# Optimization experiments

Measured on AMD Instinct MI355X. Metric: run time of the kernel, lower is better.

## Reference

```python
import jax, jax.numpy as jnp
import numpy as np

B, T, I, H, L = 32, 1024, 1024, 1024, 3


def setup_inputs() -> dict:
    key = jax.random.key(0)
    ks = jax.random.split(key, 8)
    sc_in = 1.0 / np.sqrt(I)
    sc_h = 1.0 / np.sqrt(H)
    return {
        "x": jax.random.normal(ks[0], (B, T, I), dtype=jnp.float32),
        "s0": jnp.zeros((B, H), dtype=jnp.float32),
        "w_h": jax.random.normal(ks[1], (I, H), dtype=jnp.float32) * sc_in,
        "w_t": jax.random.normal(ks[2], (I, H), dtype=jnp.float32) * sc_in,
        "w_c": jax.random.normal(ks[3], (I, H), dtype=jnp.float32) * sc_in,
        "Rh": jax.random.normal(ks[4], (L, H, H), dtype=jnp.float32) * sc_h,
        "Rt": jax.random.normal(ks[5], (L, H, H), dtype=jnp.float32) * sc_h,
        "Rc": jax.random.normal(ks[6], (L, H, H), dtype=jnp.float32) * sc_h,
        "bh": jnp.zeros((L, H), dtype=jnp.float32),
        "bt": jnp.zeros((L, H), dtype=jnp.float32),
        "bc": jnp.zeros((L, H), dtype=jnp.float32),
    }


def reference(x, s0, w_h, w_t, w_c, Rh, Rt, Rc, bh, bt, bc):
    # x: [B, T, I]; s0: [B, H]. Dropout prob = 0 -> identity.
    num_layers = Rh.shape[0]

    def step(s, x_t):
        # Input projections only feed layer 0 (as in the torch code).
        whx = x_t @ w_h  # [B, H]
        wtx = x_t @ w_t
        wcx = x_t @ w_c
        for l in range(num_layers):
            h_in = (whx if l == 0 else 0.0) + s @ Rh[l].T + bh[l]
            t_in = (wtx if l == 0 else 0.0) + s @ Rt[l].T + bt[l]
            c_in = (wcx if l == 0 else 0.0) + s @ Rc[l].T + bc[l]
            h = jnp.tanh(h_in)
            t = jax.nn.sigmoid(t_in)
            c = jax.nn.sigmoid(c_in)
            s = h * t + s * c
        return s, s

    x_tbi = jnp.swapaxes(x, 0, 1)  # [T, B, I] for scan over time
    s_T, outs = jax.lax.scan(step, s0, x_tbi)
    return jnp.swapaxes(outs, 0, 1), s_T  # ([B, T, H], [B, H])
```

## Files before the change

kernel.cpp:

```cpp
#include <hip/hip_runtime.h>
#include <hip/hip_bf16.h>

static constexpr int Bb = 32;
static constexpr int Tt = 1024;
static constexpr int Ii = 1024;
static constexpr int Hh = 1024;
static constexpr int NWG = 256;

typedef float f4 __attribute__((ext_vector_type(4)));

static constexpr int LDS_WORDS = 36 * 1024 + 4 * 12 * 32;
static constexpr int LDS_BYTES = LDS_WORDS * 4;

template <typename PT> __device__ __forceinline__ float pt_to_f(PT v);
template <> __device__ __forceinline__ float pt_to_f<float>(float v) { return v; }
template <> __device__ __forceinline__ float pt_to_f<__hip_bfloat16>(__hip_bfloat16 v) { return __bfloat162float(v); }

template <typename PT> __device__ __forceinline__ PT f_to_pt(float v);
template <> __device__ __forceinline__ float f_to_pt<float>(float v) { return v; }
template <> __device__ __forceinline__ __hip_bfloat16 f_to_pt<__hip_bfloat16>(float v) { return __float2bfloat16(v); }

#define SGLD(dst, p, lit) \
    asm volatile("global_load_dwordx4 %0, %1, off offset:" lit " sc0 sc1" : "=v"(dst) : "v"(p))
#define GB(sv, p, a,b,c,d2,e,f,g2,h) \
    SGLD(sv[0],p,a); SGLD(sv[1],p,b); SGLD(sv[2],p,c); SGLD(sv[3],p,d2); \
    SGLD(sv[4],p,e); SGLD(sv[5],p,f); SGLD(sv[6],p,g2); SGLD(sv[7],p,h)
#define VWAIT(n) do { asm volatile("s_waitcnt vmcnt(" #n ")" ::: "memory"); \
                      __builtin_amdgcn_sched_barrier(0); } while (0)

template <typename PT>
__global__ __launch_bounds__(256, 2) void proj_gemm(
    const float* __restrict__ X, const float* __restrict__ Wh,
    const float* __restrict__ Wt, const float* __restrict__ Wc,
    PT* __restrict__ P2)
{
    __shared__ float smem[4160];
    float* As = smem;
    float* Bs = smem + 1088;

    const int tid = threadIdx.x;
    const int tx = tid & 15, ty = tid >> 4;
    const int col0 = blockIdx.x * 64;
    const int t0 = blockIdx.y * 2;

    float acc[3][4][4];
#pragma unroll
    for (int g = 0; g < 3; ++g)
#pragma unroll
        for (int mm = 0; mm < 4; ++mm)
#pragma unroll
            for (int nn = 0; nn < 4; ++nn) acc[g][mm][nn] = 0.f;

    const int lm = tid >> 2, lk4 = (tid & 3) * 4;
    const float* aptr = X + ((size_t)(lm & 31) * Tt + (t0 + (lm >> 5))) * Ii + lk4;
    const int bk = tid >> 4, bn4 = (tid & 15) * 4;

    for (int k0 = 0; k0 < Ii; k0 += 16) {
        float4 av = *(const float4*)(aptr + k0);
        As[(lk4 + 0) * 68 + lm] = av.x;
        As[(lk4 + 1) * 68 + lm] = av.y;
        As[(lk4 + 2) * 68 + lm] = av.z;
        As[(lk4 + 3) * 68 + lm] = av.w;
        *(float4*)&Bs[0 * 1024 + bk * 64 + bn4] = *(const float4*)(Wh + (size_t)(k0 + bk) * Hh + col0 + bn4);
        *(float4*)&Bs[1 * 1024 + bk * 64 + bn4] = *(const float4*)(Wt + (size_t)(k0 + bk) * Hh + col0 + bn4);
        *(float4*)&Bs[2 * 1024 + bk * 64 + bn4] = *(const float4*)(Wc + (size_t)(k0 + bk) * Hh + col0 + bn4);
        __syncthreads();
#pragma unroll
        for (int k = 0; k < 16; ++k) {
            float4 a = *(const float4*)&As[k * 68 + ty * 4];
            float a_[4] = {a.x, a.y, a.z, a.w};
#pragma unroll
            for (int g = 0; g < 3; ++g) {
                float4 b = *(const float4*)&Bs[g * 1024 + k * 64 + tx * 4];
                float b_[4] = {b.x, b.y, b.z, b.w};
#pragma unroll
                for (int mm = 0; mm < 4; ++mm)
#pragma unroll
                    for (int nn = 0; nn < 4; ++nn)
                        acc[g][mm][nn] += a_[mm] * b_[nn];
            }
        }
        __syncthreads();
    }

    float* E = smem;
    const int b4 = (tid & 7) * 4;
#pragma unroll 1
    for (int g = 0; g < 3; ++g) {
        __syncthreads();
#pragma unroll
        for (int mm = 0; mm < 4; ++mm)
#pragma unroll
            for (int nn = 0; nn < 4; ++nn)
                E[(ty * 4 + mm) * 65 + tx * 4 + nn] = acc[g][mm][nn];
        __syncthreads();
        PT* dst = P2 + (size_t)g * Tt * Hh * Bb;
#pragma unroll
        for (int it = 0; it < 4; ++it) {
            const int line = (tid >> 3) + it * 32;
            const int tt = line >> 6, hh = line & 63;
            const float o0 = E[(tt * 32 + b4 + 0) * 65 + hh];
            const float o1 = E[(tt * 32 + b4 + 1) * 65 + hh];
            const float o2 = E[(tt * 32 + b4 + 2) * 65 + hh];
            const float o3 = E[(tt * 32 + b4 + 3) * 65 + hh];
            PT* d = dst + ((size_t)(t0 + tt) * Hh + col0 + hh) * Bb + b4;
            d[0] = f_to_pt<PT>(o0); d[1] = f_to_pt<PT>(o1);
            d[2] = f_to_pt<PT>(o2); d[3] = f_to_pt<PT>(o3);
        }
    }
}

__global__ void init_k(const float* __restrict__ s0, float* __restrict__ sbuf,
                       unsigned* __restrict__ flags)
{
    const int i = blockIdx.x * 256 + threadIdx.x;
    if (i < Bb * Hh) { const int b = i >> 10, h = i & 1023; sbuf[h * 32 + b] = s0[i]; }
    if (i < 256) flags[i] = 0;
}

template <typename ST>
__global__ __launch_bounds__(256) void out_transpose(
    const ST* __restrict__ shist, float* __restrict__ out, float* __restrict__ sT)
{
    __shared__ float tile[128 * 33];
    const int tid = threadIdx.x;
    const int h0 = blockIdx.x * 128;
    const int t = blockIdx.y;
    const ST* src = shist + ((size_t)t * Hh + h0) * Bb;
#pragma unroll
    for (int e = 0; e < 16; ++e) {
        const int idx = e * 256 + tid;
        tile[(idx >> 5) * 33 + (idx & 31)] = pt_to_f<ST>(src[idx]);
    }
    __syncthreads();
    const int hi = tid & 31, bq = tid >> 5;
#pragma unroll
    for (int e = 0; e < 4; ++e) {
        const int b = bq + e * 8;
        float4 v;
        v.x = tile[(hi * 4 + 0) * 33 + b];
        v.y = tile[(hi * 4 + 1) * 33 + b];
        v.z = tile[(hi * 4 + 2) * 33 + b];
        v.w = tile[(hi * 4 + 3) * 33 + b];
        *(float4*)(out + ((size_t)b * Tt + t) * Hh + h0 + hi * 4) = v;
        if (t == Tt - 1) *(float4*)(sT + (size_t)b * Hh + h0 + hi * 4) = v;
    }
}

template <typename PT, typename ST, bool DIRECT>
__global__ __launch_bounds__(256, 1) void rhn_recur(
    const float* __restrict__ Rh, const float* __restrict__ Rt,
    const float* __restrict__ Rc, const float* __restrict__ bh,
    const float* __restrict__ bt, const float* __restrict__ bc,
    const PT* __restrict__ P2, float* __restrict__ sbuf,
    unsigned* __restrict__ flags, ST* __restrict__ shist,
    float* __restrict__ out, float* __restrict__ sT)
{
    extern __shared__ float lds[];
    float* part = lds + 36 * 1024;

    const int g = blockIdx.x;
    const int tid = threadIdx.x;

    {
        const int k4 = tid * 4;
        const int sk = k4 ^ (((k4 >> 5) & 7) << 2);
#pragma unroll 1
        for (int j = 0; j < 36; ++j) {
            const int l = j / 12;
            const int rem = j - l * 12;
            const int gt = rem >> 2;
            const int q = rem & 3;
            const int h = (q << 8) | g;
            const float* src = (gt == 0 ? Rh : (gt == 1 ? Rt : Rc)) + ((size_t)l * Hh + h) * Hh;
            *(float4*)&lds[(j << 10) | sk] = *(const float4*)(src + k4);
        }
    }
    __syncthreads();

    const int ks = tid >> 3;
    const int b0 = (tid & 7) << 2;
    const int q8 = ks & 7;
    const int wv = tid >> 6;
    const int ub = tid & 31;
    const int uqc = (tid >> 5) & 3;
    const int uhc = (uqc << 8) | g;

    int o2[8];
#pragma unroll
    for (int c = 0; c < 8; ++c) o2[c] = ((c ^ q8) << 2);

    float brh[3], brt[3], brc[3];
#pragma unroll
    for (int l = 0; l < 3; ++l) {
        brh[l] = bh[l * Hh + uhc];
        brt[l] = bt[l * Hh + uhc];
        brc[l] = bc[l * Hh + uhc];
    }

    float so_reg = sbuf[uhc * 32 + ub];

    const float* sr = sbuf;
    float* sw = sbuf + Hh * Bb;

#pragma unroll 1
    for (int t = 0; t < Tt; ++t) {
#pragma unroll 1
        for (int l = 0; l < 3; ++l) {
            float pv0 = 0.f, pv1 = 0.f, pv2 = 0.f;
            if (l == 0 && tid < 128) {
                const size_t pb = ((size_t)t * Hh + uhc) * Bb + ub;
                pv0 = pt_to_f<PT>(P2[pb]);
                pv1 = pt_to_f<PT>(P2[(size_t)Tt * Hh * Bb + pb]);
                pv2 = pt_to_f<PT>(P2[2 * (size_t)Tt * Hh * Bb + pb]);
            }

            const float* sA = sr + (ks << 5) * 32 + b0;
            const float* rp = lds + l * 12288 + (ks << 5);

            f4 accv[12];
#pragma unroll
            for (int jj = 0; jj < 12; ++jj) accv[jj] = (f4){0.f, 0.f, 0.f, 0.f};

            f4 sv0[8], sv1[8];
            GB(sv0, sA, "0","128","256","384","512","640","768","896");
            GB(sv1, sA, "1024","1152","1280","1408","1536","1664","1792","1920");
            VWAIT(8);
#pragma unroll
            for (int jj = 0; jj < 12; ++jj) {
                const f4 r0 = *(const f4*)(rp + jj * 1024 + o2[0]);
                const f4 r1 = *(const f4*)(rp + jj * 1024 + o2[1]);
                f4 a = accv[jj];
                a += sv0[0] * r0[0]; a += sv0[1] * r0[1]; a += sv0[2] * r0[2]; a += sv0[3] * r0[3];
                a += sv0[4] * r1[0]; a += sv0[5] * r1[1]; a += sv0[6] * r1[2]; a += sv0[7] * r1[3];
                accv[jj] = a;
            }
            GB(sv0, sA, "2048","2176","2304","2432","2560","2688","2816","2944");
            VWAIT(8);
#pragma unroll
            for (int jj = 0; jj < 12; ++jj) {
                const f4 r0 = *(const f4*)(rp + jj * 1024 + o2[2]);
                const f4 r1 = *(const f4*)(rp + jj * 1024 + o2[3]);
                f4 a = accv[jj];
                a += sv1[0] * r0[0]; a += sv1[1] * r0[1]; a += sv1[2] * r0[2]; a += sv1[3] * r0[3];
                a += sv1[4] * r1[0]; a += sv1[5] * r1[1]; a += sv1[6] * r1[2]; a += sv1[7] * r1[3];
                accv[jj] = a;
            }
            GB(sv1, sA, "3072","3200","3328","3456","3584","3712","3840","3968");
            VWAIT(8);
#pragma unroll
            for (int jj = 0; jj < 12; ++jj) {
                const f4 r0 = *(const f4*)(rp + jj * 1024 + o2[4]);
                const f4 r1 = *(const f4*)(rp + jj * 1024 + o2[5]);
                f4 a = accv[jj];
                a += sv0[0] * r0[0]; a += sv0[1] * r0[1]; a += sv0[2] * r0[2]; a += sv0[3] * r0[3];
                a += sv0[4] * r1[0]; a += sv0[5] * r1[1]; a += sv0[6] * r1[2]; a += sv0[7] * r1[3];
                accv[jj] = a;
            }
            VWAIT(0);
#pragma unroll
            for (int jj = 0; jj < 12; ++jj) {
                const f4 r0 = *(const f4*)(rp + jj * 1024 + o2[6]);
                const f4 r1 = *(const f4*)(rp + jj * 1024 + o2[7]);
                f4 a = accv[jj];
                a += sv1[0] * r0[0]; a += sv1[1] * r0[1]; a += sv1[2] * r0[2]; a += sv1[3] * r0[3];
                a += sv1[4] * r1[0]; a += sv1[5] * r1[1]; a += sv1[6] * r1[2]; a += sv1[7] * r1[3];
                accv[jj] = a;
            }

#pragma unroll
            for (int jj = 0; jj < 12; ++jj) {
#pragma unroll
                for (int st = 8; st <= 32; st <<= 1) {
                    accv[jj][0] += __shfl_xor(accv[jj][0], st);
                    accv[jj][1] += __shfl_xor(accv[jj][1], st);
                    accv[jj][2] += __shfl_xor(accv[jj][2], st);
                    accv[jj][3] += __shfl_xor(accv[jj][3], st);
                }
            }
            f4 s1 = accv[0];
#pragma unroll
            for (int j2 = 1; j2 < 8; ++j2) if (q8 == j2) s1 = accv[j2];
            f4 s2 = accv[8];
#pragma unroll
            for (int j2 = 1; j2 < 4; ++j2) if (q8 == j2) s2 = accv[8 + j2];
            *(f4*)&part[(wv * 12 + q8) * 32 + b0] = s1;
            if (q8 < 4) *(f4*)&part[(wv * 12 + 8 + q8) * 32 + b0] = s2;
            __syncthreads();

            if (tid < 128) {
                float vals[3];
#pragma unroll
                for (int gt = 0; gt < 3; ++gt) {
                    const int jl = (gt << 2) + uqc;
                    vals[gt] = part[jl * 32 + ub] + part[(12 + jl) * 32 + ub]
                             + part[(24 + jl) * 32 + ub] + part[(36 + jl) * 32 + ub];
                }
                float bb0, bb1, bb2;
                if (l == 0)      { bb0 = brh[0]; bb1 = brt[0]; bb2 = brc[0]; }
                else if (l == 1) { bb0 = brh[1]; bb1 = brt[1]; bb2 = brc[1]; }
                else             { bb0 = brh[2]; bb1 = brt[2]; bb2 = brc[2]; }
                vals[0] += bb0; vals[1] += bb1; vals[2] += bb2;
                if (l == 0) { vals[0] += pv0; vals[1] += pv1; vals[2] += pv2; }
                const float hv = 1.f - 2.f / (1.f + __expf(2.f * vals[0]));
                const float tv = 1.f / (1.f + __expf(-vals[1]));
                const float cv = 1.f / (1.f + __expf(-vals[2]));
                const float sn = hv * tv + so_reg * cv;
                so_reg = sn;
                __hip_atomic_store(&sw[uhc * 32 + ub], sn, __ATOMIC_RELAXED, __HIP_MEMORY_SCOPE_AGENT);
                if (!DIRECT) {
                    if (l == 2) shist[((size_t)t * Hh + uhc) * Bb + ub] = f_to_pt<ST>(sn);
                } else {
                    if (l == 2) {
                        out[((size_t)ub * Tt + t) * Hh + uhc] = sn;
                        if (t == Tt - 1) sT[(size_t)ub * Hh + uhc] = sn;
                    }
                }
            }

            const unsigned ph = (unsigned)(t * 3 + l + 1);
            __syncthreads();
            if (tid == 0)
                __hip_atomic_store(&flags[g], ph, __ATOMIC_RELAXED, __HIP_MEMORY_SCOPE_AGENT);
            if (tid < 64) {
                for (;;) {
                    const unsigned v0 = __hip_atomic_load(&flags[tid],       __ATOMIC_RELAXED, __HIP_MEMORY_SCOPE_AGENT);
                    const unsigned v1 = __hip_atomic_load(&flags[tid + 64],  __ATOMIC_RELAXED, __HIP_MEMORY_SCOPE_AGENT);
                    const unsigned v2 = __hip_atomic_load(&flags[tid + 128], __ATOMIC_RELAXED, __HIP_MEMORY_SCOPE_AGENT);
                    const unsigned v3 = __hip_atomic_load(&flags[tid + 192], __ATOMIC_RELAXED, __HIP_MEMORY_SCOPE_AGENT);
                    if (__all((int)((v0 >= ph) & (v1 >= ph) & (v2 >= ph) & (v3 >= ph)))) break;
                    __builtin_amdgcn_s_sleep(2);
                }
            }
            __syncthreads();

            float* tmp = const_cast<float*>(sr);
            sr = sw;
            sw = tmp;
        }
    }
}

extern "C" void kernel_launch(void* const* d_in, const int* in_sizes, int n_in,
                              void* d_out, int out_size, void* d_ws, size_t ws_size,
                              hipStream_t stream)
{
    (void)in_sizes; (void)n_in; (void)out_size;
    const float* x  = (const float*)d_in[0];
    const float* s0 = (const float*)d_in[1];
    const float* wh = (const float*)d_in[2];
    const float* wt = (const float*)d_in[3];
    const float* wc = (const float*)d_in[4];
    const float* Rh = (const float*)d_in[5];
    const float* Rt = (const float*)d_in[6];
    const float* Rc = (const float*)d_in[7];
    const float* bh = (const float*)d_in[8];
    const float* bt = (const float*)d_in[9];
    const float* bc = (const float*)d_in[10];

    float* out = (float*)d_out;
    float* sT  = out + (size_t)Bb * Tt * Hh;

    const size_t THB  = (size_t)Tt * Hh * Bb;
    const size_t p2f  = 3 * THB * 4, p2h = 3 * THB * 2;
    const size_t shf  = THB * 4,     shh = THB * 2;
    const size_t tail = 2 * (size_t)Hh * Bb * 4 + 4096;

    char* w = (char*)d_ws;
    float* sbuf;
    unsigned* flags;

    auto finish = [&](float* sbufp, unsigned* flagsp) {
        init_k<<<128, 256, 0, stream>>>(s0, sbufp, flagsp);
    };

    if (ws_size >= p2f + shf + tail) {
        float* P2 = (float*)w;
        float* shist = (float*)(w + p2f);
        sbuf = (float*)(w + p2f + shf);
        flags = (unsigned*)((char*)sbuf + 2 * (size_t)Hh * Bb * 4);
        proj_gemm<float><<<dim3(16, 512), 256, 0, stream>>>(x, wh, wt, wc, P2);
        finish(sbuf, flags);
        hipFuncSetAttribute(reinterpret_cast<const void*>(rhn_recur<float, float, false>),
                            hipFuncAttributeMaxDynamicSharedMemorySize, LDS_BYTES);
        void* args[] = {(void*)&Rh, (void*)&Rt, (void*)&Rc, (void*)&bh, (void*)&bt, (void*)&bc,
                        (void*)&P2, (void*)&sbuf, (void*)&flags, (void*)&shist, (void*)&out, (void*)&sT};
        hipLaunchCooperativeKernel(reinterpret_cast<void*>(rhn_recur<float, float, false>),
                                   dim3(NWG), dim3(256), args, LDS_BYTES, stream);
        out_transpose<float><<<dim3(8, 1024), 256, 0, stream>>>(shist, out, sT);
    } else if (ws_size >= p2h + shf + tail) {
        __hip_bfloat16* P2 = (__hip_bfloat16*)w;
        float* shist = (float*)(w + p2h);
        sbuf = (float*)(w + p2h + shf);
        flags = (unsigned*)((char*)sbuf + 2 * (size_t)Hh * Bb * 4);
        proj_gemm<__hip_bfloat16><<<dim3(16, 512), 256, 0, stream>>>(x, wh, wt, wc, P2);
        finish(sbuf, flags);
        hipFuncSetAttribute(reinterpret_cast<const void*>(rhn_recur<__hip_bfloat16, float, false>),
                            hipFuncAttributeMaxDynamicSharedMemorySize, LDS_BYTES);
        void* args[] = {(void*)&Rh, (void*)&Rt, (void*)&Rc, (void*)&bh, (void*)&bt, (void*)&bc,
                        (void*)&P2, (void*)&sbuf, (void*)&flags, (void*)&shist, (void*)&out, (void*)&sT};
        hipLaunchCooperativeKernel(reinterpret_cast<void*>(rhn_recur<__hip_bfloat16, float, false>),
                                   dim3(NWG), dim3(256), args, LDS_BYTES, stream);
        out_transpose<float><<<dim3(8, 1024), 256, 0, stream>>>(shist, out, sT);
    } else if (ws_size >= p2h + shh + tail) {
        __hip_bfloat16* P2 = (__hip_bfloat16*)w;
        __hip_bfloat16* shist = (__hip_bfloat16*)(w + p2h);
        sbuf = (float*)(w + p2h + shh);
        flags = (unsigned*)((char*)sbuf + 2 * (size_t)Hh * Bb * 4);
        proj_gemm<__hip_bfloat16><<<dim3(16, 512), 256, 0, stream>>>(x, wh, wt, wc, P2);
        finish(sbuf, flags);
        hipFuncSetAttribute(reinterpret_cast<const void*>(rhn_recur<__hip_bfloat16, __hip_bfloat16, false>),
                            hipFuncAttributeMaxDynamicSharedMemorySize, LDS_BYTES);
        void* args[] = {(void*)&Rh, (void*)&Rt, (void*)&Rc, (void*)&bh, (void*)&bt, (void*)&bc,
                        (void*)&P2, (void*)&sbuf, (void*)&flags, (void*)&shist, (void*)&out, (void*)&sT};
        hipLaunchCooperativeKernel(reinterpret_cast<void*>(rhn_recur<__hip_bfloat16, __hip_bfloat16, false>),
                                   dim3(NWG), dim3(256), args, LDS_BYTES, stream);
        out_transpose<__hip_bfloat16><<<dim3(8, 1024), 256, 0, stream>>>(shist, out, sT);
    } else {
        __hip_bfloat16* P2 = (__hip_bfloat16*)w;
        sbuf = (float*)(w + p2h);
        flags = (unsigned*)((char*)sbuf + 2 * (size_t)Hh * Bb * 4);
        float* shist = sbuf;
        proj_gemm<__hip_bfloat16><<<dim3(16, 512), 256, 0, stream>>>(x, wh, wt, wc, P2);
        finish(sbuf, flags);
        hipFuncSetAttribute(reinterpret_cast<const void*>(rhn_recur<__hip_bfloat16, float, true>),
                            hipFuncAttributeMaxDynamicSharedMemorySize, LDS_BYTES);
        void* args[] = {(void*)&Rh, (void*)&Rt, (void*)&Rc, (void*)&bh, (void*)&bt, (void*)&bc,
                        (void*)&P2, (void*)&sbuf, (void*)&flags, (void*)&shist, (void*)&out, (void*)&sT};
        hipLaunchCooperativeKernel(reinterpret_cast<void*>(rhn_recur<__hip_bfloat16, float, true>),
                                   dim3(NWG), dim3(256), args, LDS_BYTES, stream);
    }
}
```

Baseline: 34.86 ms.

## Replace ping-pong state buffer with write-once ring so reads can use cached loads

The two-slot swapped state buffer becomes a ring holding one slot per layer-step, so each slot is written once and never overwritten. That lets the recurrent state loads drop the sc0 sc1 cache-bypass bits and use normal cached loads. The ring also serves as the output history, removing the separate shist buffer and the per-step history store. It costs a much larger workspace and depends on cached reads of freshly written slots staying coherent across workgroups.

```diff
diff --git a/kernel.cpp b/kernel.cpp
--- a/kernel.cpp
+++ b/kernel.cpp
@@ -7,6 +7,9 @@
 static constexpr int Hh = 1024;
 static constexpr int NWG = 256;
 
+static constexpr int SLOT_E = Hh * Bb;
+static constexpr int NSLOT  = 3 * Tt + 1;
+
 typedef float f4 __attribute__((ext_vector_type(4)));
 
 static constexpr int LDS_WORDS = 36 * 1024 + 4 * 12 * 32;
@@ -20,11 +23,11 @@
 template <> __device__ __forceinline__ float f_to_pt<float>(float v) { return v; }
 template <> __device__ __forceinline__ __hip_bfloat16 f_to_pt<__hip_bfloat16>(float v) { return __float2bfloat16(v); }
 
-#define SGLD(dst, p, lit) \
-    asm volatile("global_load_dwordx4 %0, %1, off offset:" lit " sc0 sc1" : "=v"(dst) : "v"(p))
+#define CGLD(dst, p, lit) \
+    asm volatile("global_load_dwordx4 %0, %1, off offset:" lit : "=v"(dst) : "v"(p))
 #define GB(sv, p, a,b,c,d2,e,f,g2,h) \
-    SGLD(sv[0],p,a); SGLD(sv[1],p,b); SGLD(sv[2],p,c); SGLD(sv[3],p,d2); \
-    SGLD(sv[4],p,e); SGLD(sv[5],p,f); SGLD(sv[6],p,g2); SGLD(sv[7],p,h)
+    CGLD(sv[0],p,a); CGLD(sv[1],p,b); CGLD(sv[2],p,c); CGLD(sv[3],p,d2); \
+    CGLD(sv[4],p,e); CGLD(sv[5],p,f); CGLD(sv[6],p,g2); CGLD(sv[7],p,h)
 #define VWAIT(n) do { asm volatile("s_waitcnt vmcnt(" #n ")" ::: "memory"); \
                       __builtin_amdgcn_sched_barrier(0); } while (0)
 
@@ -101,36 +104,37 @@
             const int tt = line >> 6, hh = line & 63;
             const float o0 = E[(tt * 32 + b4 + 0) * 65 + hh];
             const float o1 = E[(tt * 32 + b4 + 1) * 65 + hh];
-            const float o2 = E[(tt * 32 + b4 + 2) * 65 + hh];
+            const float o2v = E[(tt * 32 + b4 + 2) * 65 + hh];
             const float o3 = E[(tt * 32 + b4 + 3) * 65 + hh];
             PT* d = dst + ((size_t)(t0 + tt) * Hh + col0 + hh) * Bb + b4;
             d[0] = f_to_pt<PT>(o0); d[1] = f_to_pt<PT>(o1);
-            d[2] = f_to_pt<PT>(o2); d[3] = f_to_pt<PT>(o3);
+            d[2] = f_to_pt<PT>(o2v); d[3] = f_to_pt<PT>(o3);
         }
     }
 }
 
-__global__ void init_k(const float* __restrict__ s0, float* __restrict__ sbuf,
+template <typename RT>
+__global__ void init_k(const float* __restrict__ s0, RT* __restrict__ ring0,
                        unsigned* __restrict__ flags)
 {
     const int i = blockIdx.x * 256 + threadIdx.x;
-    if (i < Bb * Hh) { const int b = i >> 10, h = i & 1023; sbuf[h * 32 + b] = s0[i]; }
+    if (i < Bb * Hh) { const int b = i >> 10, h = i & 1023; ring0[h * 32 + b] = f_to_pt<RT>(s0[i]); }
     if (i < 256) flags[i] = 0;
 }
 
-template <typename ST>
+template <typename RT>
 __global__ __launch_bounds__(256) void out_transpose(
-    const ST* __restrict__ shist, float* __restrict__ out, float* __restrict__ sT)
+    const RT* __restrict__ ring, float* __restrict__ out, float* __restrict__ sT)
 {
     __shared__ float tile[128 * 33];
     const int tid = threadIdx.x;
     const int h0 = blockIdx.x * 128;
     const int t = blockIdx.y;
-    const ST* src = shist + ((size_t)t * Hh + h0) * Bb;
+    const RT* src = ring + (size_t)(3 * t + 3) * SLOT_E + h0 * 32;
 #pragma unroll
     for (int e = 0; e < 16; ++e) {
         const int idx = e * 256 + tid;
-        tile[(idx >> 5) * 33 + (idx & 31)] = pt_to_f<ST>(src[idx]);
+        tile[(idx >> 5) * 33 + (idx & 31)] = pt_to_f<RT>(src[idx]);
     }
     __syncthreads();
     const int hi = tid & 31, bq = tid >> 5;
@@ -147,14 +151,13 @@
     }
 }
 
-template <typename PT, typename ST, bool DIRECT>
+template <typename PT, typename RT>
 __global__ __launch_bounds__(256, 1) void rhn_recur(
     const float* __restrict__ Rh, const float* __restrict__ Rt,
     const float* __restrict__ Rc, const float* __restrict__ bh,
     const float* __restrict__ bt, const float* __restrict__ bc,
-    const PT* __restrict__ P2, float* __restrict__ sbuf,
-    unsigned* __restrict__ flags, ST* __restrict__ shist,
-    float* __restrict__ out, float* __restrict__ sT)
+    const PT* __restrict__ P2, RT* __restrict__ ring,
+    unsigned* __restrict__ flags)
 {
     extern __shared__ float lds[];
     float* part = lds + 36 * 1024;
@@ -198,15 +201,14 @@
         brc[l] = bc[l * Hh + uhc];
     }
 
-    float so_reg = sbuf[uhc * 32 + ub];
-
-    const float* sr = sbuf;
-    float* sw = sbuf + Hh * Bb;
+    float so_reg = pt_to_f<RT>(ring[uhc * 32 + ub]);
 
 #pragma unroll 1
     for (int t = 0; t < Tt; ++t) {
 #pragma unroll 1
         for (int l = 0; l < 3; ++l) {
+            const int p = t * 3 + l;
+
             float pv0 = 0.f, pv1 = 0.f, pv2 = 0.f;
             if (l == 0 && tid < 128) {
                 const size_t pb = ((size_t)t * Hh + uhc) * Bb + ub;
@@ -215,57 +217,82 @@
                 pv2 = pt_to_f<PT>(P2[2 * (size_t)Tt * Hh * Bb + pb]);
             }
 
-            const float* sA = sr + (ks << 5) * 32 + b0;
             const float* rp = lds + l * 12288 + (ks << 5);
 
             f4 accv[12];
 #pragma unroll
             for (int jj = 0; jj < 12; ++jj) accv[jj] = (f4){0.f, 0.f, 0.f, 0.f};
 
-            f4 sv0[8], sv1[8];
-            GB(sv0, sA, "0","128","256","384","512","640","768","896");
-            GB(sv1, sA, "1024","1152","1280","1408","1536","1664","1792","1920");
-            VWAIT(8);
-#pragma unroll
-            for (int jj = 0; jj < 12; ++jj) {
-                const f4 r0 = *(const f4*)(rp + jj * 1024 + o2[0]);
-                const f4 r1 = *(const f4*)(rp + jj * 1024 + o2[1]);
-                f4 a = accv[jj];
-                a += sv0[0] * r0[0]; a += sv0[1] * r0[1]; a += sv0[2] * r0[2]; a += sv0[3] * r0[3];
-                a += sv0[4] * r1[0]; a += sv0[5] * r1[1]; a += sv0[6] * r1[2]; a += sv0[7] * r1[3];
-                accv[jj] = a;
-            }
-            GB(sv0, sA, "2048","2176","2304","2432","2560","2688","2816","2944");
-            VWAIT(8);
-#pragma unroll
-            for (int jj = 0; jj < 12; ++jj) {
-                const f4 r0 = *(const f4*)(rp + jj * 1024 + o2[2]);
-                const f4 r1 = *(const f4*)(rp + jj * 1024 + o2[3]);
-                f4 a = accv[jj];
-                a += sv1[0] * r0[0]; a += sv1[1] * r0[1]; a += sv1[2] * r0[2]; a += sv1[3] * r0[3];
-                a += sv1[4] * r1[0]; a += sv1[5] * r1[1]; a += sv1[6] * r1[2]; a += sv1[7] * r1[3];
-                accv[jj] = a;
-            }
-            GB(sv1, sA, "3072","3200","3328","3456","3584","3712","3840","3968");
-            VWAIT(8);
-#pragma unroll
-            for (int jj = 0; jj < 12; ++jj) {
-                const f4 r0 = *(const f4*)(rp + jj * 1024 + o2[4]);
-                const f4 r1 = *(const f4*)(rp + jj * 1024 + o2[5]);
-                f4 a = accv[jj];
-                a += sv0[0] * r0[0]; a += sv0[1] * r0[1]; a += sv0[2] * r0[2]; a += sv0[3] * r0[3];
-                a += sv0[4] * r1[0]; a += sv0[5] * r1[1]; a += sv0[6] * r1[2]; a += sv0[7] * r1[3];
-                accv[jj] = a;
-            }
-            VWAIT(0);
-#pragma unroll
-            for (int jj = 0; jj < 12; ++jj) {
-                const f4 r0 = *(const f4*)(rp + jj * 1024 + o2[6]);
-                const f4 r1 = *(const f4*)(rp + jj * 1024 + o2[7]);
-                f4 a = accv[jj];
-                a += sv1[0] * r0[0]; a += sv1[1] * r0[1]; a += sv1[2] * r0[2]; a += sv1[3] * r0[3];
-                a += sv1[4] * r1[0]; a += sv1[5] * r1[1]; a += sv1[6] * r1[2]; a += sv1[7] * r1[3];
-                accv[jj] = a;
+            if constexpr (sizeof(RT) == 4) {
+                const float* sA = (const float*)ring + (size_t)p * SLOT_E + (ks << 5) * 32 + b0;
+                f4 sv0[8], sv1[8];
+                GB(sv0, sA, "0","128","256","384","512","640","768","896");
+                GB(sv1, sA, "1024","1152","1280","1408","1536","1664","1792","1920");
+                VWAIT(8);
+#pragma unroll
+                for (int jj = 0; jj < 12; ++jj) {
+                    const f4 r0 = *(const f4*)(rp + jj * 1024 + o2[0]);
+                    const f4 r1 = *(const f4*)(rp + jj * 1024 + o2[1]);
+                    f4 a = accv[jj];
+                    a += sv0[0] * r0[0]; a += sv0[1] * r0[1]; a += sv0[2] * r0[2]; a += sv0[3] * r0[3];
+                    a += sv0[4] * r1[0]; a += sv0[5] * r1[1]; a += sv0[6] * r1[2]; a += sv0[7] * r1[3];
+                    accv[jj] = a;
+                }
+                GB(sv0, sA, "2048","2176","2304","2432","2560","2688","2816","2944");
+                VWAIT(8);
+#pragma unroll
+                for (int jj = 0; jj < 12; ++jj) {
+                    const f4 r0 = *(const f4*)(rp + jj * 1024 + o2[2]);
+                    const f4 r1 = *(const f4*)(rp + jj * 1024 + o2[3]);
+                    f4 a = accv[jj];
+                    a += sv1[0] * r0[0]; a += sv1[1] * r0[1]; a += sv1[2] * r0[2]; a += sv1[3] * r0[3];
+                    a += sv1[4] * r1[0]; a += sv1[5] * r1[1]; a += sv1[6] * r1[2]; a += sv1[7] * r1[3];
+                    accv[jj] = a;
+                }
+                GB(sv1, sA, "3072","3200","3328","3456","3584","3712","3840","3968");
+                VWAIT(8);
+#pragma unroll
+                for (int jj = 0; jj < 12; ++jj) {
+                    const f4 r0 = *(const f4*)(rp + jj * 1024 + o2[4]);
+                    const f4 r1 = *(const f4*)(rp + jj * 1024 + o2[5]);
+                    f4 a = accv[jj];
+                    a += sv0[0] * r0[0]; a += sv0[1] * r0[1]; a += sv0[2] * r0[2]; a += sv0[3] * r0[3];
+                    a += sv0[4] * r1[0]; a += sv0[5] * r1[1]; a += sv0[6] * r1[2]; a += sv0[7] * r1[3];
+                    accv[jj] = a;
+                }
+                VWAIT(0);
+#pragma unroll
+                for (int jj = 0; jj < 12; ++jj) {
+                    const f4 r0 = *(const f4*)(rp + jj * 1024 + o2[6]);
+                    const f4 r1 = *(const f4*)(rp + jj * 1024 + o2[7]);
+                    f4 a = accv[jj];
+                    a += sv1[0] * r0[0]; a += sv1[1] * r0[1]; a += sv1[2] * r0[2]; a += sv1[3] * r0[3];
+                    a += sv1[4] * r1[0]; a += sv1[5] * r1[1]; a += sv1[6] * r1[2]; a += sv1[7] * r1[3];
+                    accv[jj] = a;
+                }
+            } else {
+                const __hip_bfloat16* sIn = (const __hip_bfloat16*)ring + (size_t)p * SLOT_E + (ks << 5) * 32 + b0;
+#pragma unroll
+                for (int blk = 0; blk < 4; ++blk) {
+                    f4 sv[8];
+#pragma unroll
+                    for (int i = 0; i < 8; ++i) {
+                        const ushort4 u = *(const ushort4*)(sIn + (blk * 8 + i) * 32);
+                        sv[i][0] = __uint_as_float((unsigned)u.x << 16);
+                        sv[i][1] = __uint_as_float((unsigned)u.y << 16);
+                        sv[i][2] = __uint_as_float((unsigned)u.z << 16);
+                        sv[i][3] = __uint_as_float((unsigned)u.w << 16);
+                    }
+#pragma unroll
+                    for (int jj = 0; jj < 12; ++jj) {
+                        const f4 r0 = *(const f4*)(rp + jj * 1024 + o2[blk * 2]);
+                        const f4 r1 = *(const f4*)(rp + jj * 1024 + o2[blk * 2 + 1]);
+                        f4 a = accv[jj];
+                        a += sv[0] * r0[0]; a += sv[1] * r0[1]; a += sv[2] * r0[2]; a += sv[3] * r0[3];
+                        a += sv[4] * r1[0]; a += sv[5] * r1[1]; a += sv[6] * r1[2]; a += sv[7] * r1[3];
+                        accv[jj] = a;
+                    }
+                }
             }
 
 #pragma unroll
@@ -307,18 +334,17 @@
                 const float cv = 1.f / (1.f + __expf(-vals[2]));
                 const float sn = hv * tv + so_reg * cv;
                 so_reg = sn;
-                __hip_atomic_store(&sw[uhc * 32 + ub], sn, __ATOMIC_RELAXED, __HIP_MEMORY_SCOPE_AGENT);
-                if (!DIRECT) {
-                    if (l == 2) shist[((size_t)t * Hh + uhc) * Bb + ub] = f_to_pt<ST>(sn);
+                RT* wp = ring + (size_t)(p + 1) * SLOT_E + uhc * 32 + ub;
+                if constexpr (sizeof(RT) == 4) {
+                    __hip_atomic_store((float*)wp, sn, __ATOMIC_RELAXED, __HIP_MEMORY_SCOPE_AGENT);
                 } else {
-                    if (l == 2) {
-                        out[((size_t)ub * Tt + t) * Hh + uhc] = sn;
-                        if (t == Tt - 1) sT[(size_t)ub * Hh + uhc] = sn;
-                    }
-                }
-            }
-
-            const unsigned ph = (unsigned)(t * 3 + l + 1);
+                    __hip_bfloat16 b16 = __float2bfloat16(sn);
+                    __hip_atomic_store((unsigned short*)wp, *(unsigned short*)&b16,
+                                       __ATOMIC_RELAXED, __HIP_MEMORY_SCOPE_AGENT);
+                }
+            }
+
+            const unsigned ph = (unsigned)(p + 1);
             __syncthreads();
             if (tid == 0)
                 __hip_atomic_store(&flags[g], ph, __ATOMIC_RELAXED, __HIP_MEMORY_SCOPE_AGENT);
@@ -333,10 +359,6 @@
                 }
             }
             __syncthreads();
-
-            float* tmp = const_cast<float*>(sr);
-            sr = sw;
-            sw = tmp;
         }
     }
 }
@@ -363,71 +385,50 @@
 
     const size_t THB  = (size_t)Tt * Hh * Bb;
     const size_t p2f  = 3 * THB * 4, p2h = 3 * THB * 2;
-    const size_t shf  = THB * 4,     shh = THB * 2;
-    const size_t tail = 2 * (size_t)Hh * Bb * 4 + 4096;
+    const size_t ringF = (size_t)NSLOT * SLOT_E * 4;
+    const size_t ringH = (size_t)NSLOT * SLOT_E * 2;
+    const size_t tail = 4096;
 
     char* w = (char*)d_ws;
-    float* sbuf;
-    unsigned* flags;
-
-    auto finish = [&](float* sbufp, unsigned* flagsp) {
-        init_k<<<128, 256, 0, stream>>>(s0, sbufp, flagsp);
-    };
-
-    if (ws_size >= p2f + shf + tail) {
+
+    if (ws_size >= p2f + ringF + tail) {
         float* P2 = (float*)w;
-        float* shist = (float*)(w + p2f);
-        sbuf = (float*)(w + p2f + shf);
-        flags = (unsigned*)((char*)sbuf + 2 * (size_t)Hh * Bb * 4);
+        float* ring = (float*)(w + p2f);
+        unsigned* flags = (unsigned*)(w + p2f + ringF);
         proj_gemm<float><<<dim3(16, 512), 256, 0, stream>>>(x, wh, wt, wc, P2);
-        finish(sbuf, flags);
-        hipFuncSetAttribute(reinterpret_cast<const void*>(rhn_recur<float, float, false>),
+        init_k<float><<<128, 256, 0, stream>>>(s0, ring, flags);
+        hipFuncSetAttribute(reinterpret_cast<const void*>(rhn_recur<float, float>),
                             hipFuncAttributeMaxDynamicSharedMemorySize, LDS_BYTES);
         void* args[] = {(void*)&Rh, (void*)&Rt, (void*)&Rc, (void*)&bh, (void*)&bt, (void*)&bc,
-                        (void*)&P2, (void*)&sbuf, (void*)&flags, (void*)&shist, (void*)&out, (void*)&sT};
-        hipLaunchCooperativeKernel(reinterpret_cast<void*>(rhn_recur<float, float, false>),
+                        (void*)&P2, (void*)&ring, (void*)&flags};
+        hipLaunchCooperativeKernel(reinterpret_cast<void*>(rhn_recur<float, float>),
                                    dim3(NWG), dim3(256), args, LDS_BYTES, stream);
-        out_transpose<float><<<dim3(8, 1024), 256, 0, stream>>>(shist, out, sT);
-    } else if (ws_size >= p2h + shf + tail) {
+        out_transpose<float><<<dim3(8, 1024), 256, 0, stream>>>(ring, out, sT);
+    } else if (ws_size >= p2h + ringF + tail) {
         __hip_bfloat16* P2 = (__hip_bfloat16*)w;
-        float* shist = (float*)(w + p2h);
-        sbuf = (float*)(w + p2h + shf);
-        flags = (unsigned*)((char*)sbuf + 2 * (size_t)Hh * Bb * 4);
+        float* ring = (float*)(w + p2h);
+        unsigned* flags = (unsigned*)(w + p2h + ringF);
         proj_gemm<__hip_bfloat16><<<dim3(16, 512), 256, 0, stream>>>(x, wh, wt, wc, P2);
-        finish(sbuf, flags);
-        hipFuncSetAttribute(reinterpret_cast<const void*>(rhn_recur<__hip_bfloat16, float, false>),
+        init_k<float><<<128, 256, 0, stream>>>(s0, ring, flags);
+        hipFuncSetAttribute(reinterpret_cast<const void*>(rhn_recur<__hip_bfloat16, float>),
                             hipFuncAttributeMaxDynamicSharedMemorySize, LDS_BYTES);
         void* args[] = {(void*)&Rh, (void*)&Rt, (void*)&Rc, (void*)&bh, (void*)&bt, (void*)&bc,
-                        (void*)&P2, (void*)&sbuf, (void*)&flags, (void*)&shist, (void*)&out, (void*)&sT};
-        hipLaunchCooperativeKernel(reinterpret_cast<void*>(rhn_recur<__hip_bfloat16, float, false>),
+                        (void*)&P2, (void*)&ring, (void*)&flags};
+        hipLaunchCooperativeKernel(reinterpret_cast<void*>(rhn_recur<__hip_bfloat16, float>),
                                    dim3(NWG), dim3(256), args, LDS_BYTES, stream);
-        out_transpose<float><<<dim3(8, 1024), 256, 0, stream>>>(shist, out, sT);
-    } else if (ws_size >= p2h + shh + tail) {
+        out_transpose<float><<<dim3(8, 1024), 256, 0, stream>>>(ring, out, sT);
+    } else {
         __hip_bfloat16* P2 = (__hip_bfloat16*)w;
-        __hip_bfloat16* shist = (__hip_bfloat16*)(w + p2h);
-        sbuf = (float*)(w + p2h + shh);
-        flags = (unsigned*)((char*)sbuf + 2 * (size_t)Hh * Bb * 4);
+        __hip_bfloat16* ring = (__hip_bfloat16*)(w + p2h);
+        unsigned* flags = (unsigned*)(w + p2h + ringH);
         proj_gemm<__hip_bfloat16><<<dim3(16, 512), 256, 0, stream>>>(x, wh, wt, wc, P2);
-        finish(sbuf, flags);
-        hipFuncSetAttribute(reinterpret_cast<const void*>(rhn_recur<__hip_bfloat16, __hip_bfloat16, false>),
+        init_k<__hip_bfloat16><<<128, 256, 0, stream>>>(s0, ring, flags);
+        hipFuncSetAttribute(reinterpret_cast<const void*>(rhn_recur<__hip_bfloat16, __hip_bfloat16>),
                             hipFuncAttributeMaxDynamicSharedMemorySize, LDS_BYTES);
         void* args[] = {(void*)&Rh, (void*)&Rt, (void*)&Rc, (void*)&bh, (void*)&bt, (void*)&bc,
-                        (void*)&P2, (void*)&sbuf, (void*)&flags, (void*)&shist, (void*)&out, (void*)&sT};
-        hipLaunchCooperativeKernel(reinterpret_cast<void*>(rhn_recur<__hip_bfloat16, __hip_bfloat16, false>),
+                        (void*)&P2, (void*)&ring, (void*)&flags};
+        hipLaunchCooperativeKernel(reinterpret_cast<void*>(rhn_recur<__hip_bfloat16, __hip_bfloat16>),
                                    dim3(NWG), dim3(256), args, LDS_BYTES, stream);
-        out_transpose<__hip_bfloat16><<<dim3(8, 1024), 256, 0, stream>>>(shist, out, sT);
-    } else {
-        __hip_bfloat16* P2 = (__hip_bfloat16*)w;
-        sbuf = (float*)(w + p2h);
-        flags = (unsigned*)((char*)sbuf + 2 * (size_t)Hh * Bb * 4);
-        float* shist = sbuf;
-        proj_gemm<__hip_bfloat16><<<dim3(16, 512), 256, 0, stream>>>(x, wh, wt, wc, P2);
-        finish(sbuf, flags);
-        hipFuncSetAttribute(reinterpret_cast<const void*>(rhn_recur<__hip_bfloat16, float, true>),
-                            hipFuncAttributeMaxDynamicSharedMemorySize, LDS_BYTES);
-        void* args[] = {(void*)&Rh, (void*)&Rt, (void*)&Rc, (void*)&bh, (void*)&bt, (void*)&bc,
-                        (void*)&P2, (void*)&sbuf, (void*)&flags, (void*)&shist, (void*)&out, (void*)&sT};
-        hipLaunchCooperativeKernel(reinterpret_cast<void*>(rhn_recur<__hip_bfloat16, float, true>),
-                                   dim3(NWG), dim3(256), args, LDS_BYTES, stream);
+        out_transpose<__hip_bfloat16><<<dim3(8, 1024), 256, 0, stream>>>(ring, out, sT);
     }
 }
```

Result: faster. 33.73 ms (-3.2%).
